# Performance work log

Measured on AMD Instinct MI355X. Metric: run time of the kernel, lower is better.

The kernel has to match this reference:

```python
import jax, jax.numpy as jnp
import numpy as np

HEADS = 8
DIM_HEAD = 64
EPS = 1e-5


def setup_inputs() -> dict:
    key = jax.random.key(0)
    k1, k2, k3, k4 = jax.random.split(key, 4)
    dim, hidden = 256, HEADS * DIM_HEAD
    x = jax.random.normal(k1, (16, dim, 64, 64), dtype=jnp.float32)
    w_qkv = jax.random.normal(k2, (hidden * 3, dim), dtype=jnp.float32) * (dim ** -0.5)
    w_out = jax.random.normal(k3, (dim, hidden), dtype=jnp.float32) * (hidden ** -0.5)
    b_out = jax.random.normal(k4, (dim,), dtype=jnp.float32) * 0.01
    g = jnp.ones((dim,), dtype=jnp.float32)
    return {"x": x, "w_qkv": w_qkv, "w_out": w_out, "b_out": b_out, "g": g}


def reference(x, w_qkv, w_out, b_out, g):
    b, c, H, W = x.shape
    n = H * W
    scale = DIM_HEAD ** -0.5
    xf = x.reshape(b, c, n)
    # 1x1 conv == channel GEMM
    qkv = jnp.einsum('oc,bcn->bon', w_qkv, xf)          # [b, 3*hidden, n]
    q, k, v = jnp.split(qkv, 3, axis=1)
    hd = (b, HEADS, DIM_HEAD, n)
    q = q.reshape(hd)
    k = k.reshape(hd)
    v = v.reshape(hd)
    q = jax.nn.softmax(q, axis=2) * scale               # softmax over head-channel d
    k = jax.nn.softmax(k, axis=3)                       # softmax over tokens n
    v = v / n
    context = jnp.einsum('bhdn,bhen->bhde', k, v)       # [b,h,d,e], d=e=DIM_HEAD
    out = jnp.einsum('bhde,bhdn->bhen', context, q)     # [b,h,e,n]
    out = out.reshape(b, HEADS * DIM_HEAD, n)
    y = jnp.einsum('oc,bcn->bon', w_out, out) + b_out[None, :, None]
    # LayerNorm over channel dim (biased var, eps for fp32)
    mean = jnp.mean(y, axis=1, keepdims=True)
    var = jnp.mean((y - mean) ** 2, axis=1, keepdims=True)
    y = (y - mean) * jax.lax.rsqrt(var + EPS) * g[None, :, None]
    return y.reshape(b, c, H, W)
```

## Files before the change

### kernel.cpp

```cpp
#include <hip/hip_runtime.h>
#include <hip/hip_bf16.h>
#include <cstddef>
#include <cstdint>


typedef __attribute__((ext_vector_type(8))) short s16x8;
typedef __attribute__((ext_vector_type(4))) float f32x4;

#define MFMA(a,b,c) __builtin_amdgcn_mfma_f32_16x16x32_bf16(a,b,c,0,0,0)

#define XT_BSTRIDE 1048576

__device__ __forceinline__ unsigned short f2bf(float f){
    union { float f; unsigned int u; } v; v.f = f;
    unsigned int u = v.u;
    unsigned int r = (u + 0x7FFFu + ((u >> 16) & 1u)) >> 16;
    return (unsigned short)r;
}
__device__ __forceinline__ float bf2f(unsigned short b){
    union { unsigned int u; float f; } v; v.u = ((unsigned int)b) << 16;
    return v.f;
}
__device__ __forceinline__ unsigned int pack2bf(float a, float b){
    __hip_bfloat162 h = __float22bfloat162_rn(make_float2(a, b));
    union { __hip_bfloat162 h; unsigned int u; } v; v.h = h;
    return v.u;
}
__device__ __forceinline__ void gload_lds16(const void* g, void* l){
    __builtin_amdgcn_global_load_lds(
        (const __attribute__((address_space(1))) unsigned int*)g,
        (__attribute__((address_space(3))) unsigned int*)l, 16, 0, 0);
}

__global__ __launch_bounds__(256)
void xprep_kernel(const float* __restrict__ x, unsigned short* __restrict__ XT)
{
    __shared__ float xt[64*68];
    const int tid = threadIdx.x;
    const int n0 = blockIdx.x * 64;
    const int c0 = blockIdx.y * 64;
    const int b  = blockIdx.z;
    {
        const int ci = tid >> 2, ng = tid & 3;
        const float* xs = x + (size_t)b*1048576 + (size_t)(c0+ci)*4096 + n0 + ng*16;
        #pragma unroll
        for (int k=0;k<4;++k){
            float4 v = *(const float4*)(xs + k*4);
            *(float4*)&xt[ci*68 + ng*16 + k*4] = v;
        }
    }
    __syncthreads();
    const int nr = tid >> 2, cg = tid & 3;
    const int n = n0 + nr;
    unsigned short* dstrow = XT + (size_t)b*XT_BSTRIDE + (size_t)n*256;
    #pragma unroll
    for (int t2=0;t2<2;++t2){
        s16x8 pk;
        #pragma unroll
        for (int j=0;j<8;++j){
            int c = cg*16 + t2*8 + j;
            pk[j] = (short)f2bf(xt[c*68 + nr]);
        }
        int blk = (((c0>>3) + cg*2 + t2) ^ (n & 7));
        *(s16x8*)(dstrow + blk*8) = pk;
    }
}

__global__ __launch_bounds__(256)
void wprep_kernel(const float* __restrict__ w, unsigned short* __restrict__ wb)
{
    int i = (blockIdx.x*256 + threadIdx.x) * 8;
    float4 a = *(const float4*)(w + i);
    float4 b = *(const float4*)(w + i + 4);
    s16x8 pk;
    pk[0]=(short)f2bf(a.x); pk[1]=(short)f2bf(a.y); pk[2]=(short)f2bf(a.z); pk[3]=(short)f2bf(a.w);
    pk[4]=(short)f2bf(b.x); pk[5]=(short)f2bf(b.y); pk[6]=(short)f2bf(b.z); pk[7]=(short)f2bf(b.w);
    *(s16x8*)(wb + i) = pk;
}

__global__ __launch_bounds__(256,2)
void kvctx_kernel(const unsigned short* __restrict__ XT, const unsigned short* __restrict__ wb,
                  float* __restrict__ Cp, float* __restrict__ Zp)
{
    extern __shared__ char smraw[];
    unsigned short* xtile = (unsigned short*)smraw;
    unsigned short* kv    = (unsigned short*)(smraw + 32768);

    const int tid = threadIdx.x;
    const int w = tid >> 6, lane = tid & 63;
    const int l15 = lane & 15, q = lane >> 4;
    const int flat = blockIdx.x;
    const int qb  = flat & 63;
    const int h   = flat >> 6;
    const int b   = qb >> 2;
    const int seg = qb & 3;
    const int bh  = b*8 + h;

    s16x8 aW[2][8];
    #pragma unroll
    for (int mf=0;mf<2;++mf){
        int rl = w*16 + l15;
        int grow = (mf==0) ? (512 + h*64 + rl) : (1024 + h*64 + rl);
        const unsigned short* wr = wb + (size_t)grow*256 + q*8;
        #pragma unroll
        for (int kc=0;kc<8;++kc)
            aW[mf][kc] = *(const s16x8*)(wr + kc*32);
    }

    f32x4 ctxacc[4];
    #pragma unroll
    for (int ef=0;ef<4;++ef) ctxacc[ef] = (f32x4){0.f,0.f,0.f,0.f};
    float zacc[4];
    #pragma unroll
    for (int i=0;i<4;++i) zacc[i]=0.f;

    const unsigned short* gsrc0 = XT + (size_t)b*XT_BSTRIDE + (size_t)(seg*1024)*256;

    {
        const unsigned short* gs = gsrc0 + w*4096 + lane*8;
        #pragma unroll
        for (int j=0;j<8;++j)
            gload_lds16(gs + j*512, &xtile[w*4096 + j*512]);
    }
    __syncthreads();

    #pragma unroll 1
    for (int t=0;t<16;++t){
        f32x4 acc[2][4];
        #pragma unroll
        for (int mf=0;mf<2;++mf)
            #pragma unroll
            for (int nf=0;nf<4;++nf) acc[mf][nf]=(f32x4){0.f,0.f,0.f,0.f};
        #pragma unroll
        for (int kc=0;kc<8;++kc){
            s16x8 bf[4];
            #pragma unroll
            for (int nf=0;nf<4;++nf){
                int nl = nf*16 + l15;
                int blk = (kc*4 + q) ^ (nl & 7);
                bf[nf] = *(const s16x8*)&xtile[nl*256 + blk*8];
            }
            #pragma unroll
            for (int mf=0;mf<2;++mf)
                #pragma unroll
                for (int nf=0;nf<4;++nf)
                    acc[mf][nf] = MFMA(aW[mf][kc], bf[nf], acc[mf][nf]);
        }
        #pragma unroll
        for (int mf=0;mf<2;++mf){
            int row = ((mf==0) ? (w*16) : (64 + w*16)) + q*4;
            #pragma unroll
            for (int nf=0;nf<4;++nf){
                int col = nf*16 + l15;
                #pragma unroll
                for (int r=0;r<4;++r){
                    float v = acc[mf][nf][r];
                    unsigned short bv;
                    if (mf == 0){
                        v = __expf(v);
                        bv = f2bf(v);
                        zacc[r] += bf2f(bv);
                    } else {
                        bv = f2bf(v);
                    }
                    kv[(row+r)*72 + col] = bv;
                }
            }
        }
        __syncthreads();
        if (t < 15){
            const unsigned short* gs = gsrc0 + (t+1)*16384 + w*4096 + lane*8;
            #pragma unroll
            for (int j=0;j<8;++j)
                gload_lds16(gs + j*512, &xtile[w*4096 + j*512]);
        }
        #pragma unroll
        for (int kf=0;kf<2;++kf){
            s16x8 aC = *(const s16x8*)&kv[(w*16 + l15)*72 + kf*32 + q*8];
            #pragma unroll
            for (int ef=0;ef<4;++ef){
                s16x8 bC = *(const s16x8*)&kv[(64 + ef*16 + l15)*72 + kf*32 + q*8];
                ctxacc[ef] = MFMA(aC, bC, ctxacc[ef]);
            }
        }
        __syncthreads();
    }

    float* cpb = Cp + (size_t)(bh*4 + seg)*4096;
    #pragma unroll
    for (int ef=0;ef<4;++ef)
        #pragma unroll
        for (int r=0;r<4;++r){
            int d = w*16 + q*4 + r;
            cpb[d*64 + ef*16 + l15] = ctxacc[ef][r];
        }
    #pragma unroll
    for (int i=0;i<4;++i){
        #pragma unroll
        for (int off=1; off<16; off<<=1)
            zacc[i] += __shfl_xor(zacc[i], off, 64);
    }
    if (l15 == 0){
        float* zpb = Zp + (size_t)(bh*4 + seg)*64;
        #pragma unroll
        for (int r=0;r<4;++r)
            zpb[w*16 + q*4 + r] = zacc[r];
    }
}

__global__ __launch_bounds__(512)
void ctxu_kernel(const float* __restrict__ Cp, const float* __restrict__ Zp,
                 const float* __restrict__ wout, unsigned short* __restrict__ U)
{
    extern __shared__ char smraw[];
    float* wl = (float*)smraw;
    float* cl = (float*)(smraw + 69632);
    const int h = blockIdx.x, b = blockIdx.y, tid = threadIdx.x;
    const int bh = b*8 + h;
    {
        const int r = tid >> 1, half = tid & 1;
        const float* wsrc = wout + (size_t)r*512 + h*64 + half*32;
        #pragma unroll
        for (int j=0;j<8;++j){
            float4 v = *(const float4*)(wsrc + j*4);
            *(float4*)&wl[r*68 + half*32 + j*4] = v;
        }
    }
    {
        const int d = tid >> 3, e0 = (tid & 7) * 8;
        float zs = 0.f;
        #pragma unroll
        for (int s=0;s<4;++s) zs += Zp[(bh*4+s)*64 + d];
        float zv = 1.f / (zs * 4096.f);
        const float* cb = Cp + (size_t)(bh*4)*4096 + d*64 + e0;
        float v[8];
        #pragma unroll
        for (int j=0;j<8;++j) v[j]=0.f;
        #pragma unroll
        for (int s=0;s<4;++s){
            float4 t0 = *(const float4*)(cb + (size_t)s*4096);
            float4 t1 = *(const float4*)(cb + (size_t)s*4096 + 4);
            v[0]+=t0.x; v[1]+=t0.y; v[2]+=t0.z; v[3]+=t0.w;
            v[4]+=t1.x; v[5]+=t1.y; v[6]+=t1.z; v[7]+=t1.w;
        }
        #pragma unroll
        for (int j=0;j<8;++j) cl[d*68 + e0 + j] = v[j] * zv;
    }
    __syncthreads();
    const int o = tid & 255, dg = tid >> 8;
    float wlr[64];
    #pragma unroll
    for (int j=0;j<16;++j){
        float4 v = *(const float4*)&wl[o*68 + j*4];
        wlr[j*4+0]=v.x; wlr[j*4+1]=v.y; wlr[j*4+2]=v.z; wlr[j*4+3]=v.w;
    }
    float outv[32];
    #pragma unroll 1
    for (int dd=0;dd<32;++dd){
        const int d = dg*32 + dd;
        float s = 0.f;
        #pragma unroll
        for (int j=0;j<16;++j){
            float4 c4 = *(const float4*)&cl[d*68 + j*4];
            s += wlr[j*4+0]*c4.x + wlr[j*4+1]*c4.y + wlr[j*4+2]*c4.z + wlr[j*4+3]*c4.w;
        }
        outv[dd] = s * 0.125f;
    }
    unsigned short* ub = U + (size_t)b*131072 + (size_t)o*512 + h*64 + dg*32;
    #pragma unroll
    for (int g4=0; g4<4; ++g4){
        uint4 pk;
        pk.x = pack2bf(outv[g4*8+0], outv[g4*8+1]);
        pk.y = pack2bf(outv[g4*8+2], outv[g4*8+3]);
        pk.z = pack2bf(outv[g4*8+4], outv[g4*8+5]);
        pk.w = pack2bf(outv[g4*8+6], outv[g4*8+7]);
        *(uint4*)(ub + g4*8) = pk;
    }
}

__global__ __launch_bounds__(512,4)
void qout_kernel(const unsigned short* __restrict__ XT, const unsigned short* __restrict__ wb,
                 const unsigned short* __restrict__ U, const float* __restrict__ bout,
                 const float* __restrict__ gg, float* __restrict__ out)
{
    extern __shared__ char smraw[];
    unsigned short* xtile = (unsigned short*)smraw;
    unsigned short* qsm   = (unsigned short*)smraw;
    float* red = (float*)(smraw + 66560);
    float* bl  = (float*)(smraw + 70656);
    float* gl  = (float*)(smraw + 71680);

    const int tid = threadIdx.x;
    const int w = tid >> 6, lane = tid & 63, l15 = lane & 15, q = lane >> 4;
    const int b = blockIdx.y;
    const int n0 = blockIdx.x * 64;

    if (tid < 256){
        bl[tid] = bout[tid];
        gl[tid] = gg[tid];
    }
    {
        const unsigned short* gs = XT + (size_t)b*XT_BSTRIDE + (size_t)n0*256 + w*2048 + lane*8;
        #pragma unroll
        for (int j=0;j<4;++j)
            gload_lds16(gs + j*512, &xtile[w*2048 + j*512]);
    }
    const unsigned short* wq = wb + (size_t)(w*64 + l15)*256 + q*8;
    s16x8 av0[4];
    #pragma unroll
    for (int mf=0;mf<4;++mf) av0[mf] = *(const s16x8*)(wq + (size_t)mf*16*256);
    __syncthreads();

    f32x4 acc[4][4];
    #pragma unroll
    for (int mf=0;mf<4;++mf)
        #pragma unroll
        for (int nf=0;nf<4;++nf) acc[mf][nf]=(f32x4){0.f,0.f,0.f,0.f};

    #pragma unroll
    for (int kc=0; kc<8; ++kc){
        s16x8 av[4];
        #pragma unroll
        for (int mf=0;mf<4;++mf)
            av[mf] = (kc == 0) ? av0[mf]
                               : *(const s16x8*)(wq + (size_t)mf*16*256 + kc*32);
        s16x8 bf[4];
        #pragma unroll
        for (int nf=0;nf<4;++nf){
            int nl = nf*16 + l15;
            int blk = (kc*4 + q) ^ (nl & 7);
            bf[nf] = *(const s16x8*)&xtile[nl*256 + blk*8];
        }
        __builtin_amdgcn_s_setprio(1);
        #pragma unroll
        for (int mf=0;mf<4;++mf)
            #pragma unroll
            for (int nf=0;nf<4;++nf)
                acc[mf][nf] = MFMA(av[mf], bf[nf], acc[mf][nf]);
        __builtin_amdgcn_s_setprio(0);
    }

    #pragma unroll
    for (int nf=0;nf<4;++nf){
        float m = -1e30f;
        #pragma unroll
        for (int mf=0;mf<4;++mf)
            #pragma unroll
            for (int r=0;r<4;++r)
                m = fmaxf(m, acc[mf][nf][r]);
        m = fmaxf(m, __shfl_xor(m, 16, 64));
        m = fmaxf(m, __shfl_xor(m, 32, 64));
        float s = 0.f;
        #pragma unroll
        for (int mf=0;mf<4;++mf)
            #pragma unroll
            for (int r=0;r<4;++r){
                float e = __expf(acc[mf][nf][r] - m);
                acc[mf][nf][r] = e;
                s += e;
            }
        s += __shfl_xor(s, 16, 64);
        s += __shfl_xor(s, 32, 64);
        float rs = 1.f / s;
        #pragma unroll
        for (int mf=0;mf<4;++mf)
            #pragma unroll
            for (int r=0;r<4;++r)
                acc[mf][nf][r] *= rs;
    }
    __syncthreads();

    #pragma unroll
    for (int mf=0;mf<4;++mf){
        int dbase = w*64 + mf*16 + q*4;
        #pragma unroll
        for (int nf=0;nf<4;++nf){
            int n = nf*16 + l15;
            unsigned int lo = pack2bf(acc[mf][nf][0], acc[mf][nf][1]);
            unsigned int hi = pack2bf(acc[mf][nf][2], acc[mf][nf][3]);
            *(uint2*)&qsm[n*520 + dbase] = make_uint2(lo, hi);
        }
    }
    const unsigned short* Ub = U + (size_t)b*131072 + (size_t)(w*32 + l15)*512 + q*8;
    s16x8 uvP[4];
    #pragma unroll
    for (int i=0;i<4;++i)
        uvP[i] = *(const s16x8*)(Ub + (size_t)(i&1)*16*512 + (i>>1)*32);
    __syncthreads();

    f32x4 yacc[2][4];
    #pragma unroll
    for (int mf=0;mf<2;++mf)
        #pragma unroll
        for (int nf=0;nf<4;++nf) yacc[mf][nf]=(f32x4){0.f,0.f,0.f,0.f};

    #pragma unroll
    for (int kc=0; kc<16; ++kc){
        s16x8 uv[2];
        #pragma unroll
        for (int mf=0;mf<2;++mf)
            uv[mf] = (kc < 2) ? uvP[(kc<<1)|mf]
                              : *(const s16x8*)(Ub + (size_t)mf*16*512 + kc*32);
        s16x8 bf[4];
        #pragma unroll
        for (int nf=0;nf<4;++nf){
            int n = nf*16 + l15;
            bf[nf] = *(const s16x8*)&qsm[n*520 + kc*32 + q*8];
        }
        __builtin_amdgcn_s_setprio(1);
        #pragma unroll
        for (int mf=0;mf<2;++mf)
            #pragma unroll
            for (int nf=0;nf<4;++nf)
                yacc[mf][nf] = MFMA(uv[mf], bf[nf], yacc[mf][nf]);
        __builtin_amdgcn_s_setprio(0);
    }

    #pragma unroll
    for (int mf=0;mf<2;++mf){
        int ob = w*32 + mf*16 + q*4;
        #pragma unroll
        for (int r=0;r<4;++r){
            float bo = bl[ob + r];
            #pragma unroll
            for (int nf=0;nf<4;++nf) yacc[mf][nf][r] += bo;
        }
    }
    float s1[4], s2[4];
    #pragma unroll
    for (int nf=0;nf<4;++nf){ s1[nf]=0.f; s2[nf]=0.f; }
    #pragma unroll
    for (int mf=0;mf<2;++mf)
        #pragma unroll
        for (int nf=0;nf<4;++nf)
            #pragma unroll
            for (int r=0;r<4;++r){
                float v = yacc[mf][nf][r];
                s1[nf] += v; s2[nf] += v*v;
            }
    #pragma unroll
    for (int nf=0;nf<4;++nf){
        s1[nf] += __shfl_xor(s1[nf], 16, 64);
        s1[nf] += __shfl_xor(s1[nf], 32, 64);
        s2[nf] += __shfl_xor(s2[nf], 16, 64);
        s2[nf] += __shfl_xor(s2[nf], 32, 64);
    }
    if (q == 0){
        #pragma unroll
        for (int nf=0;nf<4;++nf){
            int col = nf*16 + l15;
            red[(w*64 + col)*2 + 0] = s1[nf];
            red[(w*64 + col)*2 + 1] = s2[nf];
        }
    }
    __syncthreads();
    float mean_[4], inv_[4];
    #pragma unroll
    for (int nf=0;nf<4;++nf){
        int col = nf*16 + l15;
        float S1 = 0.f, S2 = 0.f;
        #pragma unroll
        for (int w2=0; w2<8; ++w2){
            S1 += red[(w2*64 + col)*2 + 0];
            S2 += red[(w2*64 + col)*2 + 1];
        }
        float mn = S1 * (1.f/256.f);
        float vr = S2 * (1.f/256.f) - mn*mn;
        mean_[nf] = mn;
        inv_[nf] = rsqrtf(vr + 1e-5f);
    }
    float* ob = out + (size_t)b*1048576 + n0;
    #pragma unroll
    for (int mf=0;mf<2;++mf){
        #pragma unroll
        for (int r=0;r<4;++r){
            int o = w*32 + mf*16 + q*4 + r;
            float gv = gl[o];
            #pragma unroll
            for (int nf=0;nf<4;++nf){
                float val = (yacc[mf][nf][r] - mean_[nf]) * inv_[nf] * gv;
                ob[(size_t)o*4096 + nf*16 + l15] = val;
            }
        }
    }
}

extern "C" void kernel_launch(void* const* d_in, const int* in_sizes, int n_in,
                              void* d_out, int out_size, void* d_ws, size_t ws_size,
                              hipStream_t stream)
{
    const float* x    = (const float*)d_in[0];
    const float* wqkv = (const float*)d_in[1];
    const float* wout = (const float*)d_in[2];
    const float* bout = (const float*)d_in[3];
    const float* g    = (const float*)d_in[4];
    float* out = (float*)d_out;

    char* wsb = (char*)d_ws;
    unsigned short* XTs = (unsigned short*)wsb;
    unsigned short* wbf = (unsigned short*)(wsb + 33554432);
    unsigned short* Ubf = (unsigned short*)(wsb + 34340864);
    float* Cp  = (float*)(wsb + 38535168);
    float* Zp  = (float*)(wsb + 46923776);

    hipLaunchKernelGGL(xprep_kernel, dim3(64, 4, 16), dim3(256), 0,     stream, x, XTs);
    hipLaunchKernelGGL(wprep_kernel, dim3(192),       dim3(256), 0,     stream, wqkv, wbf);
    hipLaunchKernelGGL(kvctx_kernel, dim3(512),       dim3(256), 51200, stream, XTs, wbf, Cp, Zp);
    hipLaunchKernelGGL(ctxu_kernel,  dim3(8, 16),     dim3(512), 87040, stream, Cp, Zp, wout, Ubf);
    hipLaunchKernelGGL(qout_kernel,  dim3(64, 16),    dim3(512), 72704, stream, XTs, wbf, Ubf, bout, g, out);
}
```

Measured before the change: 155.1 us.

## Retile qout kernel warps into 4x2 row/column grid

Replaces the per-warp tiling of the Q-projection and output GEMMs in qout_kernel. Each of the 8 warps used to own 64 rows by all 64 tokens; now warps form a 4x2 grid, each owning 128 rows (two heads) by 32 tokens in the first GEMM and 64 output rows by 32 tokens in the second. The per-head softmax and the LayerNorm reduction indices are adjusted to match. This changes the ratio of global weight loads to LDS loads per MFMA: more weight fragments per warp and fewer LDS reads. The cost is higher register pressure (8 A fragments per step), which may hurt occupancy under the 512x4 launch bounds.

```diff
diff --git a/kernel.cpp b/kernel.cpp
--- a/kernel.cpp
+++ b/kernel.cpp
@@ -292,6 +292,8 @@
 
     const int tid = threadIdx.x;
     const int w = tid >> 6, lane = tid & 63, l15 = lane & 15, q = lane >> 4;
+    const int rg = w >> 1;
+    const int cg = w & 1;
     const int b = blockIdx.y;
     const int n0 = blockIdx.x * 64;
 
@@ -305,141 +307,144 @@
         for (int j=0;j<4;++j)
             gload_lds16(gs + j*512, &xtile[w*2048 + j*512]);
     }
-    const unsigned short* wq = wb + (size_t)(w*64 + l15)*256 + q*8;
-    s16x8 av0[4];
-    #pragma unroll
-    for (int mf=0;mf<4;++mf) av0[mf] = *(const s16x8*)(wq + (size_t)mf*16*256);
-    __syncthreads();
-
-    f32x4 acc[4][4];
-    #pragma unroll
-    for (int mf=0;mf<4;++mf)
-        #pragma unroll
-        for (int nf=0;nf<4;++nf) acc[mf][nf]=(f32x4){0.f,0.f,0.f,0.f};
+    const unsigned short* wq = wb + (size_t)(rg*128 + l15)*256 + q*8;
+    s16x8 av0[8];
+    #pragma unroll
+    for (int mf=0;mf<8;++mf) av0[mf] = *(const s16x8*)(wq + (size_t)mf*16*256);
+    __syncthreads();
+
+    f32x4 acc[8][2];
+    #pragma unroll
+    for (int mf=0;mf<8;++mf)
+        #pragma unroll
+        for (int nf=0;nf<2;++nf) acc[mf][nf]=(f32x4){0.f,0.f,0.f,0.f};
 
     #pragma unroll
     for (int kc=0; kc<8; ++kc){
-        s16x8 av[4];
-        #pragma unroll
-        for (int mf=0;mf<4;++mf)
+        s16x8 av[8];
+        #pragma unroll
+        for (int mf=0;mf<8;++mf)
             av[mf] = (kc == 0) ? av0[mf]
                                : *(const s16x8*)(wq + (size_t)mf*16*256 + kc*32);
-        s16x8 bf[4];
-        #pragma unroll
-        for (int nf=0;nf<4;++nf){
-            int nl = nf*16 + l15;
+        s16x8 bf[2];
+        #pragma unroll
+        for (int nf=0;nf<2;++nf){
+            int nl = cg*32 + nf*16 + l15;
             int blk = (kc*4 + q) ^ (nl & 7);
             bf[nf] = *(const s16x8*)&xtile[nl*256 + blk*8];
         }
         __builtin_amdgcn_s_setprio(1);
         #pragma unroll
-        for (int mf=0;mf<4;++mf)
-            #pragma unroll
-            for (int nf=0;nf<4;++nf)
+        for (int mf=0;mf<8;++mf)
+            #pragma unroll
+            for (int nf=0;nf<2;++nf)
                 acc[mf][nf] = MFMA(av[mf], bf[nf], acc[mf][nf]);
         __builtin_amdgcn_s_setprio(0);
     }
 
     #pragma unroll
-    for (int nf=0;nf<4;++nf){
-        float m = -1e30f;
-        #pragma unroll
-        for (int mf=0;mf<4;++mf)
-            #pragma unroll
-            for (int r=0;r<4;++r)
-                m = fmaxf(m, acc[mf][nf][r]);
-        m = fmaxf(m, __shfl_xor(m, 16, 64));
-        m = fmaxf(m, __shfl_xor(m, 32, 64));
-        float s = 0.f;
-        #pragma unroll
-        for (int mf=0;mf<4;++mf)
-            #pragma unroll
-            for (int r=0;r<4;++r){
-                float e = __expf(acc[mf][nf][r] - m);
-                acc[mf][nf][r] = e;
-                s += e;
-            }
-        s += __shfl_xor(s, 16, 64);
-        s += __shfl_xor(s, 32, 64);
-        float rs = 1.f / s;
-        #pragma unroll
-        for (int mf=0;mf<4;++mf)
-            #pragma unroll
-            for (int r=0;r<4;++r)
-                acc[mf][nf][r] *= rs;
-    }
-    __syncthreads();
-
-    #pragma unroll
-    for (int mf=0;mf<4;++mf){
-        int dbase = w*64 + mf*16 + q*4;
-        #pragma unroll
-        for (int nf=0;nf<4;++nf){
-            int n = nf*16 + l15;
+    for (int hh=0;hh<2;++hh){
+        #pragma unroll
+        for (int nf=0;nf<2;++nf){
+            float m = -1e30f;
+            #pragma unroll
+            for (int mf=0;mf<4;++mf)
+                #pragma unroll
+                for (int r=0;r<4;++r)
+                    m = fmaxf(m, acc[hh*4+mf][nf][r]);
+            m = fmaxf(m, __shfl_xor(m, 16, 64));
+            m = fmaxf(m, __shfl_xor(m, 32, 64));
+            float s = 0.f;
+            #pragma unroll
+            for (int mf=0;mf<4;++mf)
+                #pragma unroll
+                for (int r=0;r<4;++r){
+                    float e = __expf(acc[hh*4+mf][nf][r] - m);
+                    acc[hh*4+mf][nf][r] = e;
+                    s += e;
+                }
+            s += __shfl_xor(s, 16, 64);
+            s += __shfl_xor(s, 32, 64);
+            float rs = 1.f / s;
+            #pragma unroll
+            for (int mf=0;mf<4;++mf)
+                #pragma unroll
+                for (int r=0;r<4;++r)
+                    acc[hh*4+mf][nf][r] *= rs;
+        }
+    }
+    __syncthreads();
+
+    #pragma unroll
+    for (int mf=0;mf<8;++mf){
+        int dbase = rg*128 + mf*16 + q*4;
+        #pragma unroll
+        for (int nf=0;nf<2;++nf){
+            int n = cg*32 + nf*16 + l15;
             unsigned int lo = pack2bf(acc[mf][nf][0], acc[mf][nf][1]);
             unsigned int hi = pack2bf(acc[mf][nf][2], acc[mf][nf][3]);
             *(uint2*)&qsm[n*520 + dbase] = make_uint2(lo, hi);
         }
     }
-    const unsigned short* Ub = U + (size_t)b*131072 + (size_t)(w*32 + l15)*512 + q*8;
+    const unsigned short* Ub = U + (size_t)b*131072 + (size_t)(rg*64 + l15)*512 + q*8;
     s16x8 uvP[4];
     #pragma unroll
     for (int i=0;i<4;++i)
-        uvP[i] = *(const s16x8*)(Ub + (size_t)(i&1)*16*512 + (i>>1)*32);
-    __syncthreads();
-
-    f32x4 yacc[2][4];
-    #pragma unroll
-    for (int mf=0;mf<2;++mf)
-        #pragma unroll
-        for (int nf=0;nf<4;++nf) yacc[mf][nf]=(f32x4){0.f,0.f,0.f,0.f};
+        uvP[i] = *(const s16x8*)(Ub + (size_t)i*16*512);
+    __syncthreads();
+
+    f32x4 yacc[4][2];
+    #pragma unroll
+    for (int mf=0;mf<4;++mf)
+        #pragma unroll
+        for (int nf=0;nf<2;++nf) yacc[mf][nf]=(f32x4){0.f,0.f,0.f,0.f};
 
     #pragma unroll
     for (int kc=0; kc<16; ++kc){
-        s16x8 uv[2];
-        #pragma unroll
-        for (int mf=0;mf<2;++mf)
-            uv[mf] = (kc < 2) ? uvP[(kc<<1)|mf]
-                              : *(const s16x8*)(Ub + (size_t)mf*16*512 + kc*32);
-        s16x8 bf[4];
-        #pragma unroll
-        for (int nf=0;nf<4;++nf){
-            int n = nf*16 + l15;
+        s16x8 uv[4];
+        #pragma unroll
+        for (int mf=0;mf<4;++mf)
+            uv[mf] = (kc == 0) ? uvP[mf]
+                               : *(const s16x8*)(Ub + (size_t)mf*16*512 + kc*32);
+        s16x8 bf[2];
+        #pragma unroll
+        for (int nf=0;nf<2;++nf){
+            int n = cg*32 + nf*16 + l15;
             bf[nf] = *(const s16x8*)&qsm[n*520 + kc*32 + q*8];
         }
         __builtin_amdgcn_s_setprio(1);
         #pragma unroll
-        for (int mf=0;mf<2;++mf)
-            #pragma unroll
-            for (int nf=0;nf<4;++nf)
+        for (int mf=0;mf<4;++mf)
+            #pragma unroll
+            for (int nf=0;nf<2;++nf)
                 yacc[mf][nf] = MFMA(uv[mf], bf[nf], yacc[mf][nf]);
         __builtin_amdgcn_s_setprio(0);
     }
 
     #pragma unroll
-    for (int mf=0;mf<2;++mf){
-        int ob = w*32 + mf*16 + q*4;
+    for (int mf=0;mf<4;++mf){
+        int ob = rg*64 + mf*16 + q*4;
         #pragma unroll
         for (int r=0;r<4;++r){
             float bo = bl[ob + r];
             #pragma unroll
-            for (int nf=0;nf<4;++nf) yacc[mf][nf][r] += bo;
-        }
-    }
-    float s1[4], s2[4];
-    #pragma unroll
-    for (int nf=0;nf<4;++nf){ s1[nf]=0.f; s2[nf]=0.f; }
-    #pragma unroll
-    for (int mf=0;mf<2;++mf)
-        #pragma unroll
-        for (int nf=0;nf<4;++nf)
+            for (int nf=0;nf<2;++nf) yacc[mf][nf][r] += bo;
+        }
+    }
+    float s1[2], s2[2];
+    #pragma unroll
+    for (int nf=0;nf<2;++nf){ s1[nf]=0.f; s2[nf]=0.f; }
+    #pragma unroll
+    for (int mf=0;mf<4;++mf)
+        #pragma unroll
+        for (int nf=0;nf<2;++nf)
             #pragma unroll
             for (int r=0;r<4;++r){
                 float v = yacc[mf][nf][r];
                 s1[nf] += v; s2[nf] += v*v;
             }
     #pragma unroll
-    for (int nf=0;nf<4;++nf){
+    for (int nf=0;nf<2;++nf){
         s1[nf] += __shfl_xor(s1[nf], 16, 64);
         s1[nf] += __shfl_xor(s1[nf], 32, 64);
         s2[nf] += __shfl_xor(s2[nf], 16, 64);
@@ -447,37 +452,37 @@
     }
     if (q == 0){
         #pragma unroll
-        for (int nf=0;nf<4;++nf){
-            int col = nf*16 + l15;
-            red[(w*64 + col)*2 + 0] = s1[nf];
-            red[(w*64 + col)*2 + 1] = s2[nf];
-        }
-    }
-    __syncthreads();
-    float mean_[4], inv_[4];
-    #pragma unroll
-    for (int nf=0;nf<4;++nf){
-        int col = nf*16 + l15;
+        for (int nf=0;nf<2;++nf){
+            int col = cg*32 + nf*16 + l15;
+            red[(rg*64 + col)*2 + 0] = s1[nf];
+            red[(rg*64 + col)*2 + 1] = s2[nf];
+        }
+    }
+    __syncthreads();
+    float mean_[2], inv_[2];
+    #pragma unroll
+    for (int nf=0;nf<2;++nf){
+        int col = cg*32 + nf*16 + l15;
         float S1 = 0.f, S2 = 0.f;
         #pragma unroll
-        for (int w2=0; w2<8; ++w2){
-            S1 += red[(w2*64 + col)*2 + 0];
-            S2 += red[(w2*64 + col)*2 + 1];
+        for (int g=0; g<4; ++g){
+            S1 += red[(g*64 + col)*2 + 0];
+            S2 += red[(g*64 + col)*2 + 1];
         }
         float mn = S1 * (1.f/256.f);
         float vr = S2 * (1.f/256.f) - mn*mn;
         mean_[nf] = mn;
         inv_[nf] = rsqrtf(vr + 1e-5f);
     }
-    float* ob = out + (size_t)b*1048576 + n0;
-    #pragma unroll
-    for (int mf=0;mf<2;++mf){
+    float* ob = out + (size_t)b*1048576 + n0 + cg*32;
+    #pragma unroll
+    for (int mf=0;mf<4;++mf){
         #pragma unroll
         for (int r=0;r<4;++r){
-            int o = w*32 + mf*16 + q*4 + r;
+            int o = rg*64 + mf*16 + q*4 + r;
             float gv = gl[o];
             #pragma unroll
-            for (int nf=0;nf<4;++nf){
+            for (int nf=0;nf<2;++nf){
                 float val = (yacc[mf][nf][r] - mean_[nf]) * inv_[nf] * gv;
                 ob[(size_t)o*4096 + nf*16 + l15] = val;
             }
```

After: 212.3 us. 1.37x slower.
